# Kernel tuning notes

Hardware: AMD Instinct MI355X
Metric: run time of the kernel (lower is better)

The kernel has to match this reference:

```python
import jax, jax.numpy as jnp
import numpy as np

HIDDEN = 256
HEADS = 4
HEAD_DIM = HIDDEN // HEADS
TOPK_RATIO = 0.1
TEMP = 1.0
M = 256          # num messages
L = 64           # tokens per message (uniform, contiguous)
T = M * L        # total tokens
NB = 8           # conversations/batches
K_TARGETS = 10   # min(10, T)
NEG = -1e30      # stand-in for -inf (safe for softmax grads)


def _lin(k, out_d, in_d):
    return jax.random.normal(k, (out_d, in_d), jnp.float32) * 0.02


def setup_inputs() -> dict:
    key = jax.random.key(0)
    ks = jax.random.split(key, 10)
    starts = jnp.arange(M, dtype=jnp.int32) * L
    message_boundaries = jnp.stack([starts, starts + L], axis=1)
    batch_indices = jnp.sort(jax.random.randint(ks[0], (M,), 0, NB, dtype=jnp.int32))
    token_features = jax.random.normal(ks[1], (T, HIDDEN), jnp.float32)
    return {
        "token_features": token_features,
        "message_boundaries": message_boundaries,
        "batch_indices": batch_indices,
        "Wq": _lin(ks[2], HIDDEN, HIDDEN), "bq": jnp.zeros((HIDDEN,), jnp.float32),
        "Wk": _lin(ks[3], HIDDEN, HIDDEN), "bk": jnp.zeros((HIDDEN,), jnp.float32),
        "Wv": _lin(ks[4], HIDDEN, HIDDEN), "bv": jnp.zeros((HIDDEN,), jnp.float32),
        "Wi1": _lin(ks[5], HIDDEN // 2, HIDDEN), "bi1": jnp.zeros((HIDDEN // 2,), jnp.float32),
        "Wi2": _lin(ks[6], 1, HIDDEN // 2), "bi2": jnp.zeros((1,), jnp.float32),
        "Wo": _lin(ks[7], HIDDEN, HIDDEN), "bo": jnp.zeros((HIDDEN,), jnp.float32),
    }


def reference(token_features, message_boundaries, batch_indices,
              Wq, bq, Wk, bk, Wv, bv, Wi1, bi1, Wi2, bi2, Wo, bo):
    T_, D = token_features.shape
    Mn = message_boundaries.shape[0]
    Ln = T_ // Mn                       # uniform message length
    kk = max(1, int(Ln * TOPK_RATIO))   # per-message top-k (static)

    # importance scorer MLP -> per-token score [T]
    h = jax.nn.relu(token_features @ Wi1.T + bi1)
    imp = (h @ Wi2.T + bi2)[:, 0]

    # per-message top-k token selection (messages are contiguous spans)
    starts = message_boundaries[:, 0]
    _, idx_local = jax.lax.top_k(imp.reshape(Mn, Ln), kk)        # [M, kk]
    selected = (starts[:, None] + idx_local).reshape(-1)          # [B]
    msg_ids = jnp.repeat(jnp.arange(Mn), kk)                      # [B]
    token_msg_ids = jnp.searchsorted(starts, jnp.arange(T_), side='right') - 1  # [T]

    # projections
    q = (token_features[selected] @ Wq.T + bq).reshape(-1, HEADS, HEAD_DIM)  # [B,H,d]
    kmat = (token_features @ Wk.T + bk).reshape(T_, HEADS, HEAD_DIM)         # [T,H,d]
    vmat = (token_features @ Wv.T + bv).reshape(T_, HEADS, HEAD_DIM)         # [T,H,d]

    scores = jnp.einsum('bhd,thd->bht', q, kmat) / (HEAD_DIM ** 0.5 * TEMP)  # [B,H,T]

    # mask: only attend to tokens in a DIFFERENT message but SAME batch
    diff_msg = msg_ids[:, None] != token_msg_ids[None, :]
    same_batch = batch_indices[msg_ids][:, None] == batch_indices[token_msg_ids][None, :]
    valid = diff_msg & same_batch                                  # [B,T]
    scores = jnp.where(valid[:, None, :], scores, NEG)

    # top-k targets per (query, head), softmax, gather values
    kt = min(K_TARGETS, T_)
    top_scores, top_idx = jax.lax.top_k(scores, kt)                # [B,H,kt]
    w = jax.nn.softmax(top_scores, axis=-1)
    gathered = vmat[top_idx, jnp.arange(HEADS)[None, :, None], :]  # [B,H,kt,d]
    attended = jnp.einsum('bhk,bhkd->bhd', w, gathered).reshape(-1, D)

    updates = attended @ Wo.T + bo                                 # [B,D]
    updated = token_features.at[selected].add(updates)             # scatter-add (indices unique)
    avg_scores = top_scores.mean(axis=1)                           # [B,kt]
    return updated, avg_scores
```

## Files before the change

kernel.cpp:

```cpp
#include <hip/hip_runtime.h>
#include <math.h>

#define T_TOK 16384
#define M_MSG 256
#define L_TOK 64
#define KK 6
#define NQ (M_MSG * KK)
#define D_HID 256
#define NH 4
#define HD 64
#define KT 10
#define NBATCH 8

__device__ __forceinline__ unsigned ordf(float f) {
  unsigned u = __float_as_uint(f);
  return (u & 0x80000000u) ? ~u : (u | 0x80000000u);
}
__device__ __forceinline__ float unordf(unsigned u) {
  return __uint_as_float((u & 0x80000000u) ? (u ^ 0x80000000u) : ~u);
}

typedef _Float16 h2v __attribute__((ext_vector_type(2)));
typedef _Float16 h8v __attribute__((ext_vector_type(8)));
typedef float f4v __attribute__((ext_vector_type(4)));
typedef __fp16 fp16x2 __attribute__((ext_vector_type(2)));
__device__ __forceinline__ h2v u2h(unsigned u) {
  return __builtin_bit_cast(h2v, u);
}
__device__ __forceinline__ unsigned pkh(float a, float b) {
  fp16x2 h = __builtin_amdgcn_cvt_pkrtz(a, b);
  return __builtin_bit_cast(unsigned, h);
}
#if defined(__has_builtin) && __has_builtin(__builtin_amdgcn_fdot2)
__device__ __forceinline__ float FDOT2(h2v a, h2v b, float c) {
  return __builtin_amdgcn_fdot2(a, b, c, false);
}
#else
__device__ __forceinline__ float FDOT2(h2v a, h2v b, float c) {
  return c + (float)a.x * (float)b.x + (float)a.y * (float)b.y;
}
#endif

__global__ __launch_bounds__(64) void wpanel_kernel(
    const float* __restrict__ Wk, const float* __restrict__ Wv,
    const float* __restrict__ Wq, const float* __restrict__ Wo,
    const float* __restrict__ Wi1, uint4* __restrict__ WkH,
    uint4* __restrict__ WvH, float4* __restrict__ WqP,
    float4* __restrict__ WoP, float4* __restrict__ Wi1P) {
  int c = blockIdx.x;
  int t = threadIdx.x;
  WqP[t * 256 + c] = ((const float4*)(Wq + (size_t)c * 256))[t];
  WoP[t * 256 + c] = ((const float4*)(Wo + (size_t)c * 256))[t];
  if (c < 128) Wi1P[t * 128 + c] = ((const float4*)(Wi1 + (size_t)c * 256))[t];
  const float* Wsrc = (t < 32) ? Wk : Wv;
  uint4* dst = (t < 32) ? WkH : WvH;
  int d8 = t & 31;
  float4 a = ((const float4*)(Wsrc + (size_t)c * 256))[d8 * 2];
  float4 b = ((const float4*)(Wsrc + (size_t)c * 256))[d8 * 2 + 1];
  uint4 p;
  p.x = pkh(a.x, a.y);
  p.y = pkh(a.z, a.w);
  p.z = pkh(b.x, b.y);
  p.w = pkh(b.z, b.w);
  dst[d8 * 256 + c] = p;
}

__global__ __launch_bounds__(256) void kvimp_kernel(
    const float* __restrict__ X, const uint4* __restrict__ WkH,
    const float* __restrict__ bk, const uint4* __restrict__ WvH,
    const float* __restrict__ bv, const float4* __restrict__ Wi1P,
    const float* __restrict__ bi1, const float* __restrict__ Wi2,
    const float* __restrict__ bi2, unsigned* __restrict__ Kout,
    float* __restrict__ Vout, float* __restrict__ imp) {
  __shared__ float xs[32][260];
  __shared__ float partial[4][16];
  int tid = threadIdx.x;
  if (blockIdx.x < 1024) {
    int r0 = blockIdx.x * 16;
    unsigned* xh = (unsigned*)&xs[0][0];
    const float4* Xv = (const float4*)(X + (size_t)r0 * 256);
#pragma unroll
    for (int i = 0; i < 2; ++i) {
      int n = i * 256 + tid;
      int row = n >> 5, d8 = n & 31;
      float4 a = Xv[row * 64 + d8 * 2];
      float4 b = Xv[row * 64 + d8 * 2 + 1];
      uint4 p;
      p.x = pkh(a.x, a.y);
      p.y = pkh(a.z, a.w);
      p.z = pkh(b.x, b.y);
      p.w = pkh(b.z, b.w);
      ((uint4*)(xh + row * 132))[d8] = p;
    }
    __syncthreads();
    int lane = tid & 63, w = tid >> 6;
    int mat = w >> 1;
    int cbase = (w & 1) * 128;
    int arow = lane & 15, akg = lane >> 4;
    const uint4* P = mat ? WvH : WkH;
    uint4 a8[8];
#pragma unroll
    for (int kb = 0; kb < 8; ++kb)
      a8[kb] = ((const uint4*)xh)[arow * 33 + kb * 4 + akg];
#pragma unroll
    for (int tt = 0; tt < 8; ++tt) {
      int c0 = cbase + tt * 16;
      f4v acc = {0.f, 0.f, 0.f, 0.f};
#pragma unroll
      for (int kb = 0; kb < 8; ++kb) {
        uint4 b = P[(size_t)(kb * 4 + akg) * 256 + c0 + arow];
        acc = __builtin_amdgcn_mfma_f32_16x16x32_f16(
            __builtin_bit_cast(h8v, a8[kb]), __builtin_bit_cast(h8v, b), acc,
            0, 0, 0);
      }
      int col = c0 + arow;
      if (mat == 0) {
        float bb = bk[col];
#pragma unroll
        for (int r = 0; r < 4; ++r)
          xs[16 + akg * 4 + r][col] = acc[r] + bb;
      } else {
        float bb = bv[col];
#pragma unroll
        for (int r = 0; r < 4; ++r)
          Vout[(size_t)(r0 + akg * 4 + r) * 256 + col] = acc[r] + bb;
      }
    }
    __syncthreads();
    uint4* Kbv = (uint4*)Kout;
#pragma unroll
    for (int i = 0; i < 2; ++i) {
      int idx = i * 256 + tid;
      int hd8 = idx >> 4;
      int r = idx & 15;
      const float* row = &xs[16 + r][hd8 * 8];
      uint4 p;
      p.x = pkh(row[0], row[1]);
      p.y = pkh(row[2], row[3]);
      p.z = pkh(row[4], row[5]);
      p.w = pkh(row[6], row[7]);
      Kbv[(size_t)hd8 * T_TOK + r0 + r] = p;
    }
  } else {
    int t0 = (blockIdx.x - 1024) * 32;
    const float4* Xv = (const float4*)(X + (size_t)t0 * 256);
    for (int n = tid; n < 2048; n += 256) {
      int row = n >> 6, sl = n & 63;
      ((float4*)xs[row])[sl] = Xv[row * 64 + sl];
    }
    __syncthreads();
    int j = tid & 127, grp = tid >> 7;
    float acc[16];
#pragma unroll
    for (int tt = 0; tt < 16; ++tt) acc[tt] = 0.f;
    for (int i4 = 0; i4 < 64; ++i4) {
      float4 w = Wi1P[i4 * 128 + j];
#pragma unroll
      for (int tt = 0; tt < 16; ++tt) {
        float4 x = ((const float4*)xs[grp * 16 + tt])[i4];
        acc[tt] += x.x * w.x + x.y * w.y + x.z * w.z + x.w * w.w;
      }
    }
    float b1 = bi1[j], w2 = Wi2[j];
    float p[16];
#pragma unroll
    for (int tt = 0; tt < 16; ++tt) {
      float hh = acc[tt] + b1;
      hh = hh > 0.f ? hh : 0.f;
      p[tt] = hh * w2;
    }
#pragma unroll
    for (int s = 1; s < 64; s <<= 1) {
#pragma unroll
      for (int tt = 0; tt < 16; ++tt) p[tt] += __shfl_xor(p[tt], s, 64);
    }
    int lane = tid & 63, wv_ = tid >> 6;
    if (lane == 0) {
#pragma unroll
      for (int tt = 0; tt < 16; ++tt) partial[wv_][tt] = p[tt];
    }
    __syncthreads();
    if (tid < 32) {
      int g = tid >> 4, tt = tid & 15;
      imp[t0 + g * 16 + tt] =
          partial[2 * g][tt] + partial[2 * g + 1][tt] + bi2[0];
    }
  }
}

__global__ __launch_bounds__(256) void topselq_kernel(
    const float* __restrict__ imp, const int* __restrict__ mb,
    const int* __restrict__ bidx, const float* __restrict__ X,
    const float4* __restrict__ WqP, const float* __restrict__ bq,
    int* __restrict__ selected, int* __restrict__ lo, int* __restrict__ hi,
    float* __restrict__ Qout) {
  int m = blockIdx.x;
  int tid = threadIdx.x;
  if (m == M_MSG) {
    int g = tid;
    if (g < NBATCH) {
      int l = 0;
      while (l < M_MSG && bidx[l] < g) ++l;
      int h = l;
      while (h < M_MSG && bidx[h] == g) ++h;
      lo[g] = l * L_TOK;
      hi[g] = h * L_TOK;
    }
    return;
  }
  __shared__ int sel[KK];
  __shared__ float4 xs6[KK][64];
  if (tid < 64) {
    int l = tid;
    float myv = imp[m * 64 + l];
    int start = mb[2 * m];
    for (int k = 0; k < KK; ++k) {
      float rv = myv;
      int ri = l;
#pragma unroll
      for (int s = 1; s < 64; s <<= 1) {
        float ov = __shfl_xor(rv, s, 64);
        int oi = __shfl_xor(ri, s, 64);
        if (ov > rv || (ov == rv && oi < ri)) { rv = ov; ri = oi; }
      }
      if (l == 0) {
        selected[m * KK + k] = start + ri;
        sel[k] = start + ri;
      }
      if (l == ri) myv = -INFINITY;
    }
  }
  __syncthreads();
  for (int i = tid; i < KK * 64; i += 256) {
    int r = i >> 6, d4 = i & 63;
    xs6[r][d4] = ((const float4*)X)[(size_t)sel[r] * 64 + d4];
  }
  __syncthreads();
  float acc[KK];
#pragma unroll
  for (int r = 0; r < KK; ++r) acc[r] = 0.f;
  for (int i4 = 0; i4 < 64; ++i4) {
    float4 w = WqP[i4 * 256 + tid];
#pragma unroll
    for (int r = 0; r < KK; ++r) {
      float4 x = xs6[r][i4];
      acc[r] += x.x * w.x + x.y * w.y + x.z * w.z + x.w * w.w;
    }
  }
  float bj = bq[tid];
#pragma unroll
  for (int r = 0; r < KK; ++r)
    Qout[(size_t)(m * KK + r) * 256 + tid] = (acc[r] + bj) * 0.125f;
}

__global__ __launch_bounds__(128) void scores_kernel(
    const float* __restrict__ Q, const unsigned* __restrict__ Kb,
    const int* __restrict__ lo_, const int* __restrict__ hi_,
    const int* __restrict__ bidx, unsigned long long* __restrict__ topk2) {
  int bid = blockIdx.x;
  int sw = (bid & 7) * (M_MSG * NH * 2 / 8) + (bid >> 3);
  int m = sw >> 3;
  int h = (sw >> 1) & 3;
  int sp = sw & 1;
  int tid = threadIdx.x, lane = tid & 63, w = tid >> 6;
  int g = bidx[m];
  int lo = lo_[g], hi = hi_[g];
  int range = hi - lo;
  int n_all = (range + 63) >> 6;
  int n0 = (n_all + 1) >> 1;
  int nt = sp ? (n_all - n0) : n0;
  int start = lo + (sp ? n0 * 64 : 0);
  int end0 = lo + n0 * 64;
  int end = sp ? hi : (end0 < hi ? end0 : hi);

  __shared__ uint4 qh[KK][8];
  const float4* Qv = (const float4*)Q;
  for (int i = tid; i < KK * 8; i += 128) {
    int qq = i >> 3, d8 = i & 7;
    float4 a = Qv[(size_t)(m * KK + qq) * 64 + h * 16 + d8 * 2];
    float4 b = Qv[(size_t)(m * KK + qq) * 64 + h * 16 + d8 * 2 + 1];
    uint4 p;
    p.x = pkh(a.x, a.y);
    p.y = pkh(a.z, a.w);
    p.z = pkh(b.x, b.y);
    p.w = pkh(b.z, b.w);
    qh[qq][d8] = p;
  }
  __syncthreads();

  unsigned long long lst[3][KT];
#pragma unroll
  for (int j = 0; j < 3; ++j)
#pragma unroll
    for (int k = 0; k < KT; ++k) lst[j][k] = 0ULL;

  const uint4* Kh = (const uint4*)Kb + (size_t)h * 8 * T_TOK;

#pragma unroll 1
  for (int kb = 0; kb < nt; ++kb) {
    int t = start + kb * 64 + lane;
    int tc = t < hi ? t : hi - 1;
    uint4 kw[8];
#pragma unroll
    for (int d8 = 0; d8 < 8; ++d8) kw[d8] = Kh[(size_t)d8 * T_TOK + tc];
    float acc[3];
    acc[0] = 0.f; acc[1] = 0.f; acc[2] = 0.f;
#pragma unroll
    for (int d8 = 0; d8 < 8; ++d8) {
      uint4 kv = kw[d8];
#pragma unroll
      for (int j = 0; j < 3; ++j) {
        uint4 qv = qh[w * 3 + j][d8];
        float a = acc[j];
        a = FDOT2(u2h(kv.x), u2h(qv.x), a);
        a = FDOT2(u2h(kv.y), u2h(qv.y), a);
        a = FDOT2(u2h(kv.z), u2h(qv.z), a);
        a = FDOT2(u2h(kv.w), u2h(qv.w), a);
        acc[j] = a;
      }
    }
    bool v0 = (t < end) && ((t >> 6) != m);
    unsigned nk = ~(unsigned)t;
#pragma unroll
    for (int j = 0; j < 3; ++j) {
      unsigned cc = v0 ? ordf(acc[j]) : 0u;
      unsigned long long key =
          cc ? (((unsigned long long)cc << 32) | nk) : 0ULL;
      if (key > lst[j][KT - 1]) {
        unsigned long long ins = key;
#pragma unroll
        for (int r = 0; r < KT; ++r) {
          unsigned long long cur = lst[j][r];
          unsigned long long mx = ins > cur ? ins : cur;
          unsigned long long mn = ins > cur ? cur : ins;
          lst[j][r] = mx;
          ins = mn;
        }
      }
    }
  }

  for (int k = 0; k < KT; ++k) {
    unsigned long long mx[3];
#pragma unroll
    for (int j = 0; j < 3; ++j) mx[j] = lst[j][0];
#pragma unroll
    for (int s_ = 1; s_ < 64; s_ <<= 1) {
#pragma unroll
      for (int j = 0; j < 3; ++j) {
        unsigned long long o = __shfl_xor(mx[j], s_, 64);
        if (o > mx[j]) mx[j] = o;
      }
    }
#pragma unroll
    for (int j = 0; j < 3; ++j) {
      if (mx[j] != 0ULL && lst[j][0] == mx[j]) {
#pragma unroll
        for (int r = 0; r < KT - 1; ++r) lst[j][r] = lst[j][r + 1];
        lst[j][KT - 1] = 0ULL;
      }
    }
    if (lane == 0) {
#pragma unroll
      for (int j = 0; j < 3; ++j) {
        int q = m * KK + w * 3 + j;
        topk2[((size_t)(q * NH + h) * 2 + sp) * KT + k] = mx[j];
      }
    }
  }
}

__global__ __launch_bounds__(256) void finish_kernel(
    const unsigned long long* __restrict__ topk2, const float* __restrict__ V,
    const float4* __restrict__ WoP, const float* __restrict__ bo,
    const int* __restrict__ selected, float* __restrict__ out,
    float* __restrict__ out_avg) {
  int q0 = blockIdx.x * 4;
  int tid = threadIdx.x;
  __shared__ unsigned long long buf[16][2 * KT];
  __shared__ float tvs[4][NH][KT];
  __shared__ int tis[4][NH][KT];
  __shared__ float wsm[4][NH * KT];
  __shared__ float att[4][256];
  const unsigned long long* src = topk2 + (size_t)q0 * NH * 2 * KT;
  for (int i = tid; i < 16 * 2 * KT; i += 256) (&buf[0][0])[i] = src[i];
  __syncthreads();
  if (tid < 16) {
    int qq = tid >> 2, h = tid & 3;
    int pa = 0, pb = 0;
    float e[KT];
    float m0 = 0.f, sum = 0.f;
#pragma unroll
    for (int k = 0; k < KT; ++k) {
      unsigned long long va = buf[tid][pa];
      unsigned long long vb = buf[tid][KT + pb];
      unsigned long long v;
      if (va >= vb) { v = va; ++pa; } else { v = vb; ++pb; }
      float scv;
      int t;
      if (v != 0ULL) {
        scv = unordf((unsigned)(v >> 32));
        t = (int)(~(unsigned)v);
      } else {
        scv = -1e30f;
        t = 0;
      }
      tvs[qq][h][k] = scv;
      tis[qq][h][k] = t;
      if (k == 0) m0 = scv;
      e[k] = expf(scv - m0);
      sum += e[k];
    }
    float inv = 1.f / sum;
#pragma unroll
    for (int k = 0; k < KT; ++k) wsm[qq][h * KT + k] = e[k] * inv;
  }
  __syncthreads();
  if (tid < 40) {
    int qq = tid / 10, k = tid % 10;
    out_avg[(size_t)(q0 + qq) * KT + k] =
        0.25f * (tvs[qq][0][k] + tvs[qq][1][k] + tvs[qq][2][k] + tvs[qq][3][k]);
  }
  int h = tid >> 6, d = tid & 63;
#pragma unroll 1
  for (int qq = 0; qq < 4; ++qq) {
    float a = 0.f;
#pragma unroll
    for (int k = 0; k < KT; ++k) {
      int t = tis[qq][h][k];
      a += wsm[qq][h * KT + k] * V[(size_t)t * 256 + h * 64 + d];
    }
    att[qq][tid] = a;
  }
  __syncthreads();
  float acc[4];
#pragma unroll
  for (int tt = 0; tt < 4; ++tt) acc[tt] = 0.f;
  for (int i4 = 0; i4 < 64; ++i4) {
    float4 wv = WoP[i4 * 256 + tid];
#pragma unroll
    for (int tt = 0; tt < 4; ++tt) {
      float4 x = ((const float4*)att[tt])[i4];
      acc[tt] += x.x * wv.x + x.y * wv.y + x.z * wv.z + x.w * wv.w;
    }
  }
  float bj = bo[tid];
#pragma unroll 1
  for (int tt = 0; tt < 4; ++tt) {
    int s = selected[q0 + tt];
    out[(size_t)s * 256 + tid] += acc[tt] + bj;
  }
}

extern "C" void kernel_launch(void* const* d_in, const int* in_sizes, int n_in,
                              void* d_out, int out_size, void* d_ws, size_t ws_size,
                              hipStream_t stream) {
  const float* X   = (const float*)d_in[0];
  const int*   mb  = (const int*)d_in[1];
  const int*   bidx= (const int*)d_in[2];
  const float* Wq  = (const float*)d_in[3];
  const float* bq  = (const float*)d_in[4];
  const float* Wk  = (const float*)d_in[5];
  const float* bk  = (const float*)d_in[6];
  const float* Wv  = (const float*)d_in[7];
  const float* bv  = (const float*)d_in[8];
  const float* Wi1 = (const float*)d_in[9];
  const float* bi1 = (const float*)d_in[10];
  const float* Wi2 = (const float*)d_in[11];
  const float* bi2 = (const float*)d_in[12];
  const float* Wo  = (const float*)d_in[13];
  const float* bo  = (const float*)d_in[14];

  float* out = (float*)d_out;
  float* out_avg = out + (size_t)T_TOK * D_HID;

  unsigned* Kmat = (unsigned*)out;

  char* ws = (char*)d_ws;
  size_t off = 0;
  float* V = (float*)(ws + off);        off += (size_t)T_TOK * 256 * 4;
  float* Q = (float*)(ws + off);        off += (size_t)NQ * 256 * 4;
  float* imp = (float*)(ws + off);      off += (size_t)T_TOK * 4;
  int* selected = (int*)(ws + off);     off += (size_t)NQ * 4;
  int* lo = (int*)(ws + off);           off += 64;
  int* hi = (int*)(ws + off);           off += 64;
  unsigned long long* topk2 = (unsigned long long*)(ws + off);
  off += (size_t)NQ * NH * 2 * KT * 8;
  uint4* WkH = (uint4*)(ws + off);      off += (size_t)32 * 256 * 16;
  uint4* WvH = (uint4*)(ws + off);      off += (size_t)32 * 256 * 16;
  float4* WqP = (float4*)(ws + off);    off += (size_t)64 * 256 * 16;
  float4* WoP = (float4*)(ws + off);    off += (size_t)64 * 256 * 16;
  float4* Wi1P = (float4*)(ws + off);   off += (size_t)64 * 128 * 16;
  (void)ws_size; (void)in_sizes; (void)n_in; (void)out_size;

  wpanel_kernel<<<256, 64, 0, stream>>>(Wk, Wv, Wq, Wo, Wi1, WkH, WvH, WqP,
                                        WoP, Wi1P);
  kvimp_kernel<<<1536, 256, 0, stream>>>(X, WkH, bk, WvH, bv, Wi1P, bi1, Wi2,
                                         bi2, Kmat, V, imp);
  topselq_kernel<<<M_MSG + 1, 256, 0, stream>>>(imp, mb, bidx, X, WqP, bq,
                                                selected, lo, hi, Q);
  scores_kernel<<<M_MSG * NH * 2, 128, 0, stream>>>(Q, Kmat, lo, hi, bidx,
                                                    topk2);
  hipMemcpyAsync(out, X, (size_t)T_TOK * D_HID * sizeof(float),
                 hipMemcpyDeviceToDevice, stream);
  finish_kernel<<<NQ / 4, 256, 0, stream>>>(topk2, V, WoP, bo, selected, out,
                                            out_avg);
}
```

Baseline: 186.2 us.

## Compute attention scores with MFMA and split key range across waves

Replaces the per-lane packed-half dot products in the scores kernel with 16x16x32 f16 MFMA instructions, computing scores for 16 keys by 16 query columns (6 used) per instruction pair. Each of the two waves now takes half of the key range, and each lane keeps a single top-k list instead of three. The finish kernel merges four partial lists per query/head instead of two, and the workspace for partial top-k grows to match. The goal is to cut ALU cost in the score loop. In exchange, 10 of the 16 MFMA query columns are wasted, and the merge and writeback traffic roughly doubles.

```diff
diff --git a/kernel.cpp b/kernel.cpp
--- a/kernel.cpp
+++ b/kernel.cpp
@@ -268,10 +268,11 @@
   int range = hi - lo;
   int n_all = (range + 63) >> 6;
   int n0 = (n_all + 1) >> 1;
-  int nt = sp ? (n_all - n0) : n0;
-  int start = lo + (sp ? n0 * 64 : 0);
-  int end0 = lo + n0 * 64;
-  int end = sp ? hi : (end0 < hi ? end0 : hi);
+  int nt_sp = sp ? (n_all - n0) : n0;
+  int start_sp = lo + (sp ? n0 * 64 : 0);
+  int ntw0 = (nt_sp + 1) >> 1;
+  int nt = w ? (nt_sp - ntw0) : ntw0;
+  int start = start_sp + (w ? ntw0 * 64 : 0);
 
   __shared__ uint4 qh[KK][8];
   const float4* Qv = (const float4*)Q;
@@ -288,84 +289,72 @@
   }
   __syncthreads();
 
-  unsigned long long lst[3][KT];
-#pragma unroll
-  for (int j = 0; j < 3; ++j)
-#pragma unroll
-    for (int k = 0; k < KT; ++k) lst[j][k] = 0ULL;
+  int qcol = lane & 15;
+  int grp = lane >> 4;
+  int qcl = qcol < KK ? qcol : KK - 1;
+  uint4 bf0 = qh[qcl][grp];
+  uint4 bf1 = qh[qcl][4 + grp];
+  bool qvalid = qcol < KK;
+
+  unsigned long long lst[KT];
+#pragma unroll
+  for (int k = 0; k < KT; ++k) lst[k] = 0ULL;
 
   const uint4* Kh = (const uint4*)Kb + (size_t)h * 8 * T_TOK;
 
 #pragma unroll 1
   for (int kb = 0; kb < nt; ++kb) {
-    int t = start + kb * 64 + lane;
-    int tc = t < hi ? t : hi - 1;
-    uint4 kw[8];
-#pragma unroll
-    for (int d8 = 0; d8 < 8; ++d8) kw[d8] = Kh[(size_t)d8 * T_TOK + tc];
-    float acc[3];
-    acc[0] = 0.f; acc[1] = 0.f; acc[2] = 0.f;
-#pragma unroll
-    for (int d8 = 0; d8 < 8; ++d8) {
-      uint4 kv = kw[d8];
-#pragma unroll
-      for (int j = 0; j < 3; ++j) {
-        uint4 qv = qh[w * 3 + j][d8];
-        float a = acc[j];
-        a = FDOT2(u2h(kv.x), u2h(qv.x), a);
-        a = FDOT2(u2h(kv.y), u2h(qv.y), a);
-        a = FDOT2(u2h(kv.z), u2h(qv.z), a);
-        a = FDOT2(u2h(kv.w), u2h(qv.w), a);
-        acc[j] = a;
-      }
-    }
-    bool v0 = (t < end) && ((t >> 6) != m);
-    unsigned nk = ~(unsigned)t;
-#pragma unroll
-    for (int j = 0; j < 3; ++j) {
-      unsigned cc = v0 ? ordf(acc[j]) : 0u;
-      unsigned long long key =
-          cc ? (((unsigned long long)cc << 32) | nk) : 0ULL;
-      if (key > lst[j][KT - 1]) {
-        unsigned long long ins = key;
-#pragma unroll
-        for (int r = 0; r < KT; ++r) {
-          unsigned long long cur = lst[j][r];
-          unsigned long long mx = ins > cur ? ins : cur;
-          unsigned long long mn = ins > cur ? cur : ins;
-          lst[j][r] = mx;
-          ins = mn;
+    int tb = start + kb * 64;
+#pragma unroll
+    for (int tt = 0; tt < 4; ++tt) {
+      int ta = tb + tt * 16 + qcol;
+      int tca = ta < hi ? ta : hi - 1;
+      uint4 a0 = Kh[(size_t)(0 * 4 + grp) * T_TOK + tca];
+      uint4 a1 = Kh[(size_t)(1 * 4 + grp) * T_TOK + tca];
+      f4v acc = {0.f, 0.f, 0.f, 0.f};
+      acc = __builtin_amdgcn_mfma_f32_16x16x32_f16(
+          __builtin_bit_cast(h8v, a0), __builtin_bit_cast(h8v, bf0), acc,
+          0, 0, 0);
+      acc = __builtin_amdgcn_mfma_f32_16x16x32_f16(
+          __builtin_bit_cast(h8v, a1), __builtin_bit_cast(h8v, bf1), acc,
+          0, 0, 0);
+      int k0 = tb + tt * 16 + grp * 4;
+#pragma unroll
+      for (int r = 0; r < 4; ++r) {
+        int t = k0 + r;
+        bool v0 = qvalid && (t < hi) && ((t >> 6) != m);
+        unsigned cc = v0 ? ordf(acc[r]) : 0u;
+        unsigned long long key =
+            cc ? (((unsigned long long)cc << 32) | (unsigned)(~t)) : 0ULL;
+        if (key > lst[KT - 1]) {
+          unsigned long long ins = key;
+#pragma unroll
+          for (int rr = 0; rr < KT; ++rr) {
+            unsigned long long cur = lst[rr];
+            unsigned long long mx = ins > cur ? ins : cur;
+            unsigned long long mn = ins > cur ? cur : ins;
+            lst[rr] = mx;
+            ins = mn;
+          }
         }
       }
     }
   }
 
   for (int k = 0; k < KT; ++k) {
-    unsigned long long mx[3];
-#pragma unroll
-    for (int j = 0; j < 3; ++j) mx[j] = lst[j][0];
-#pragma unroll
-    for (int s_ = 1; s_ < 64; s_ <<= 1) {
-#pragma unroll
-      for (int j = 0; j < 3; ++j) {
-        unsigned long long o = __shfl_xor(mx[j], s_, 64);
-        if (o > mx[j]) mx[j] = o;
-      }
-    }
-#pragma unroll
-    for (int j = 0; j < 3; ++j) {
-      if (mx[j] != 0ULL && lst[j][0] == mx[j]) {
-#pragma unroll
-        for (int r = 0; r < KT - 1; ++r) lst[j][r] = lst[j][r + 1];
-        lst[j][KT - 1] = 0ULL;
-      }
-    }
-    if (lane == 0) {
-#pragma unroll
-      for (int j = 0; j < 3; ++j) {
-        int q = m * KK + w * 3 + j;
-        topk2[((size_t)(q * NH + h) * 2 + sp) * KT + k] = mx[j];
-      }
+    unsigned long long mx = lst[0];
+    unsigned long long o = __shfl_xor(mx, 16, 64);
+    if (o > mx) mx = o;
+    o = __shfl_xor(mx, 32, 64);
+    if (o > mx) mx = o;
+    if (mx != 0ULL && lst[0] == mx) {
+#pragma unroll
+      for (int r = 0; r < KT - 1; ++r) lst[r] = lst[r + 1];
+      lst[KT - 1] = 0ULL;
+    }
+    if (lane < KK) {
+      int q = m * KK + lane;
+      topk2[((size_t)(q * NH + h) * 4 + sp * 2 + w) * KT + k] = mx;
     }
   }
 }
@@ -377,25 +366,32 @@
     float* __restrict__ out_avg) {
   int q0 = blockIdx.x * 4;
   int tid = threadIdx.x;
-  __shared__ unsigned long long buf[16][2 * KT];
+  __shared__ unsigned long long buf[16][4 * KT];
   __shared__ float tvs[4][NH][KT];
   __shared__ int tis[4][NH][KT];
   __shared__ float wsm[4][NH * KT];
   __shared__ float att[4][256];
-  const unsigned long long* src = topk2 + (size_t)q0 * NH * 2 * KT;
-  for (int i = tid; i < 16 * 2 * KT; i += 256) (&buf[0][0])[i] = src[i];
+  const unsigned long long* src = topk2 + (size_t)q0 * NH * 4 * KT;
+  for (int i = tid; i < 16 * 4 * KT; i += 256) (&buf[0][0])[i] = src[i];
   __syncthreads();
   if (tid < 16) {
     int qq = tid >> 2, h = tid & 3;
-    int pa = 0, pb = 0;
+    int pa = 0, pb = 0, pc = 0, pd = 0;
     float e[KT];
     float m0 = 0.f, sum = 0.f;
 #pragma unroll
     for (int k = 0; k < KT; ++k) {
       unsigned long long va = buf[tid][pa];
       unsigned long long vb = buf[tid][KT + pb];
-      unsigned long long v;
-      if (va >= vb) { v = va; ++pa; } else { v = vb; ++pb; }
+      unsigned long long vc = buf[tid][2 * KT + pc];
+      unsigned long long vd = buf[tid][3 * KT + pd];
+      unsigned long long m1 = va >= vb ? va : vb;
+      unsigned long long m2 = vc >= vd ? vc : vd;
+      unsigned long long v = m1 >= m2 ? m1 : m2;
+      if (v == va) ++pa;
+      else if (v == vb) ++pb;
+      else if (v == vc) ++pc;
+      else ++pd;
       float scv;
       int t;
       if (v != 0ULL) {
@@ -485,7 +481,7 @@
   int* lo = (int*)(ws + off);           off += 64;
   int* hi = (int*)(ws + off);           off += 64;
   unsigned long long* topk2 = (unsigned long long*)(ws + off);
-  off += (size_t)NQ * NH * 2 * KT * 8;
+  off += (size_t)NQ * NH * 4 * KT * 8;
   uint4* WkH = (uint4*)(ws + off);      off += (size_t)32 * 256 * 16;
   uint4* WvH = (uint4*)(ws + off);      off += (size_t)32 * 256 * 16;
   float4* WqP = (float4*)(ws + off);    off += (size_t)64 * 256 * 16;
```

Result: slower. 209.8 us (+12.6%).
